# Optimization experiments

Hardware: AMD Instinct MI355X
Metric: run time of the kernel (lower is better)

The kernel has to match this reference:

```python
import jax, jax.numpy as jnp
import numpy as np

N_NODES = 200000
MAX_DEG = 128
S1, S2 = 25, 10  # neighbor sample sizes per hop (GraphSAGE defaults)


def setup_inputs() -> dict:
    key = jax.random.key(0)
    ks = jax.random.split(key, 9)
    F, H, C, B = 256, 128, 41, 1024
    return {
        "node_ids": jax.random.randint(ks[0], (B,), 0, N_NODES, dtype=jnp.int32),
        "features": jax.random.normal(ks[1], (N_NODES, F), dtype=jnp.float32),
        "adj_info": jax.random.randint(ks[2], (N_NODES, MAX_DEG), 0, N_NODES, dtype=jnp.int32),
        "W_self1": jax.random.normal(ks[3], (F, H), dtype=jnp.float32) * 0.05,
        "W_neigh1": jax.random.normal(ks[4], (F, H), dtype=jnp.float32) * 0.05,
        "W_self2": jax.random.normal(ks[5], (2 * H, H), dtype=jnp.float32) * 0.05,
        "W_neigh2": jax.random.normal(ks[6], (2 * H, H), dtype=jnp.float32) * 0.05,
        "W_pred": jax.random.normal(ks[7], (2 * H, C), dtype=jnp.float32) * 0.05,
        "b_pred": jnp.zeros((C,), dtype=jnp.float32),
    }


def _sample(adj_info, node_ids):
    """Uniform neighbor sampling: hop1 [B,S1], hop2 [B,S1,S2]."""
    k1, k2 = jax.random.split(jax.random.key(42))
    B = node_ids.shape[0]
    cols1 = jax.random.randint(k1, (B, S1), 0, MAX_DEG)
    hop1 = jnp.take_along_axis(adj_info[node_ids], cols1, axis=1)  # [B,S1]
    cols2 = jax.random.randint(k2, (B * S1, S2), 0, MAX_DEG)
    hop2 = jnp.take_along_axis(adj_info[hop1.reshape(-1)], cols2, axis=1)
    return hop1, hop2.reshape(B, S1, S2)


def _mean_agg(self_f, neigh_f, Ws, Wn, act):
    # GraphSAGE MeanAggregator with concat: [self@Ws ; mean(neigh)@Wn]
    neigh = neigh_f.mean(axis=-2)
    return act(jnp.concatenate([self_f @ Ws, neigh @ Wn], axis=-1))


def reference(node_ids, features, adj_info, W_self1, W_neigh1, W_self2, W_neigh2, W_pred, b_pred):
    hop1, hop2 = _sample(adj_info, node_ids)
    f0 = features[node_ids]      # [B,F]
    f1 = features[hop1]          # [B,S1,F]
    f2 = features[hop2]          # [B,S1,S2,F]

    h0 = _mean_agg(f0, f1, W_self1, W_neigh1, jax.nn.relu)   # [B,2H]
    h1 = _mean_agg(f1, f2, W_self1, W_neigh1, jax.nn.relu)   # [B,S1,2H]
    h = _mean_agg(h0, h1, W_self2, W_neigh2, lambda x: x)    # [B,2H]

    # tf.math.l2_normalize(x, 1): x * rsqrt(max(sum(x^2), 1e-12))
    h = h * jax.lax.rsqrt(jnp.maximum(jnp.sum(h * h, axis=1, keepdims=True), 1e-12))
    logits = h @ W_pred + b_pred
    return jax.nn.softmax(logits, axis=-1)
```

## Files before the change

### kernel.cpp

```cpp
#include <hip/hip_runtime.h>
#include <cstdint>
#include <cstddef>

#define BATCH 1024
#define S1 25
#define S2 10
#define FDIM 256
#define HDIM 128
#define NCLS 41
#define MAXDEG 128

typedef __attribute__((ext_vector_type(8))) short bf16x8;
typedef __attribute__((ext_vector_type(4))) float f32x4;

__host__ __device__ static inline void tf2x32(uint32_t k0, uint32_t k1,
                                              uint32_t c0, uint32_t c1,
                                              uint32_t& o0, uint32_t& o1) {
  const uint32_t ks2 = k0 ^ k1 ^ 0x1BD11BDAu;
  uint32_t x0 = c0 + k0, x1 = c1 + k1;
#define TFR(r) { x0 += x1; x1 = (x1 << (r)) | (x1 >> (32 - (r))); x1 ^= x0; }
  TFR(13) TFR(15) TFR(26) TFR(6)
  x0 += k1;  x1 += ks2 + 1u;
  TFR(17) TFR(29) TFR(16) TFR(24)
  x0 += ks2; x1 += k0 + 2u;
  TFR(13) TFR(15) TFR(26) TFR(6)
  x0 += k0;  x1 += k1 + 3u;
  TFR(17) TFR(29) TFR(16) TFR(24)
  x0 += k1;  x1 += ks2 + 4u;
  TFR(13) TFR(15) TFR(26) TFR(6)
  x0 += ks2; x1 += k0 + 5u;
#undef TFR
  o0 = x0; o1 = x1;
}

__device__ static inline uint32_t rand_bits_at(uint32_t kb0, uint32_t kb1, uint32_t j) {
  uint32_t o0, o1;
  tf2x32(kb0, kb1, 0u, j, o0, o1);
  return o0 ^ o1;
}

__device__ static inline ushort f2bf(float x) {
  uint32_t u = __float_as_uint(x);
  return (ushort)((u + 0x7fffu + ((u >> 16) & 1u)) >> 16);
}

__global__ __launch_bounds__(256)
void wprep_kernel(const float* __restrict__ Ws1, const float* __restrict__ Wn1,
                  ushort* __restrict__ WbT) {
  const int idx = blockIdx.x;
  const int h = idx >> 7, n = idx & 127;
  const float* W = h ? Wn1 : Ws1;
  WbT[(size_t)idx * FDIM + threadIdx.x] = f2bf(W[(size_t)threadIdx.x * HDIM + n]);
}

__global__ __launch_bounds__(256, 3)
void mega_kernel(const int* __restrict__ node_ids, const float* __restrict__ feat,
                 const int* __restrict__ adj, const ushort* __restrict__ WbT,
                 const float* __restrict__ Ws1, const float* __restrict__ Wn1,
                 const float* __restrict__ Ws2, const float* __restrict__ Wn2,
                 const float* __restrict__ Wp, const float* __restrict__ bp,
                 float* __restrict__ out,
                 uint32_t kb1_0, uint32_t kb1_1, uint32_t kb2_0, uint32_t kb2_1) {
  const int b = blockIdx.x;
  const int t = threadIdx.x;
  const int wave = t >> 6, lane = t & 63;
  const int lq = lane >> 4, lr = lane & 15;

  __shared__ int    hop1s[S1];
  __shared__ int    hop2s[S1 * S2];
  __shared__ ushort As0[8][32][40];
  __shared__ ushort As1[8][32][40];
  __shared__ float  F0[FDIM];
  __shared__ float  N1[4][FDIM];
  __shared__ float  H1M[2 * HDIM];
  __shared__ float  H0[2 * HDIM];
  __shared__ float  HN[2 * HDIM];
  __shared__ float  red[4];
  __shared__ float  lg[NCLS];
  __shared__ float  smx[2];

  const int nid = node_ids[b];

  if (t < S1) {
    uint32_t c1 = rand_bits_at(kb1_0, kb1_1, (uint32_t)(b * S1 + t)) & (MAXDEG - 1);
    hop1s[t] = adj[(size_t)nid * MAXDEG + c1];
  }
  __syncthreads();

  if (t < S1 * S2) {
    const int s1 = t / S2, j = t - s1 * S2;
    uint32_t c2 = rand_bits_at(kb2_0, kb2_1, (uint32_t)((b * S1 + s1) * S2 + j)) & (MAXDEG - 1);
    hop2s[t] = adj[(size_t)hop1s[s1] * MAXDEG + c2];
  }
  if (t < 64) ((float4*)F0)[t] = ((const float4*)(feat + (size_t)nid * FDIM))[t];
  {
    ushort4 z; z.x = 0; z.y = 0; z.z = 0; z.w = 0;
    for (int i = t; i < 448; i += 256) {
      const int rc = i >> 3, q = i & 7;
      const int r = 25 + (rc >> 3), ch = rc & 7;
      *(ushort4*)&As0[ch][r][q * 4] = z;
      *(ushort4*)&As1[ch][r][q * 4] = z;
    }
  }
  __syncthreads();

  {
    float ax = 0.f, ay = 0.f, az = 0.f, aw = 0.f;
    for (int s1 = wave; s1 < S1; s1 += 4) {
      const int rid1 = hop1s[s1];
      float4 v = ((const float4*)(feat + (size_t)rid1 * FDIM))[lane];
      float bx = 0.f, by = 0.f, bz = 0.f, bw = 0.f;
#pragma unroll
      for (int r = 0; r < S2; ++r) {
        const int rid = hop2s[s1 * S2 + r];
        float4 w = ((const float4*)(feat + (size_t)rid * FDIM))[lane];
        bx += w.x; by += w.y; bz += w.z; bw += w.w;
      }
      ax += v.x; ay += v.y; az += v.z; aw += v.w;
      ushort4 o1;
      o1.x = f2bf(v.x); o1.y = f2bf(v.y); o1.z = f2bf(v.z); o1.w = f2bf(v.w);
      *(ushort4*)&As0[lane >> 3][s1][(lane & 7) * 4] = o1;
      const float inv2 = 1.f / S2;
      ushort4 o2;
      o2.x = f2bf(bx * inv2); o2.y = f2bf(by * inv2);
      o2.z = f2bf(bz * inv2); o2.w = f2bf(bw * inv2);
      *(ushort4*)&As1[lane >> 3][s1][(lane & 7) * 4] = o2;
    }
    float4 p; p.x = ax; p.y = ay; p.z = az; p.w = aw;
    ((float4*)N1[wave])[lane] = p;
  }
  __syncthreads();

  {
    const float s = N1[0][t] + N1[1][t] + N1[2][t] + N1[3][t];
    N1[0][t] = s * (1.f / S1);
  }

#pragma unroll 1
  for (int half = 0; half < 2; ++half) {
    const ushort* Bmat = WbT + (size_t)half * HDIM * FDIM;
    const ushort (*As)[32][40] = half ? As1 : As0;

    bf16x8 bfr[2][8];
#pragma unroll
    for (int ct = 0; ct < 2; ++ct)
#pragma unroll
      for (int k0 = 0; k0 < 8; ++k0)
        bfr[ct][k0] = *(const bf16x8*)(Bmat + (size_t)(wave * 32 + ct * 16 + lr) * FDIM
                                       + k0 * 32 + lq * 8);

    f32x4 acc[2][2];
#pragma unroll
    for (int rt = 0; rt < 2; ++rt)
#pragma unroll
      for (int ct = 0; ct < 2; ++ct) acc[rt][ct] = (f32x4)(0.f);

#pragma unroll
    for (int k0 = 0; k0 < 8; ++k0) {
      bf16x8 af0 = *(const bf16x8*)&As[k0][lr][lq * 8];
      bf16x8 af1 = *(const bf16x8*)&As[k0][16 + lr][lq * 8];
#pragma unroll
      for (int ct = 0; ct < 2; ++ct) {
        acc[0][ct] = __builtin_amdgcn_mfma_f32_16x16x32_bf16(af0, bfr[ct][k0], acc[0][ct], 0, 0, 0);
        acc[1][ct] = __builtin_amdgcn_mfma_f32_16x16x32_bf16(af1, bfr[ct][k0], acc[1][ct], 0, 0, 0);
      }
    }

#pragma unroll
    for (int ct = 0; ct < 2; ++ct) {
      float s = 0.f;
#pragma unroll
      for (int rt = 0; rt < 2; ++rt)
#pragma unroll
        for (int r = 0; r < 4; ++r)
          s += fmaxf(acc[rt][ct][r], 0.f);
      s += __shfl_xor(s, 16, 64);
      s += __shfl_xor(s, 32, 64);
      if (lq == 0) H1M[half * HDIM + wave * 32 + ct * 16 + lr] = s * (1.f / S1);
    }
  }
  __syncthreads();

  const int hh = t >> 7, c = t & 127;
  {
    const float* W = hh ? Wn1 : Ws1;
    const float* Ap = hh ? N1[0] : F0;
    float acc = 0.f;
#pragma unroll 4
    for (int k4 = 0; k4 < 64; ++k4) {
      float4 a = ((const float4*)Ap)[k4];
      acc += a.x * W[(size_t)(k4 * 4 + 0) * HDIM + c]
           + a.y * W[(size_t)(k4 * 4 + 1) * HDIM + c]
           + a.z * W[(size_t)(k4 * 4 + 2) * HDIM + c]
           + a.w * W[(size_t)(k4 * 4 + 3) * HDIM + c];
    }
    H0[t] = fmaxf(acc, 0.f);
  }
  __syncthreads();

  float hv;
  {
    const float* W = hh ? Wn2 : Ws2;
    const float* Ap = hh ? H1M : H0;
    float acc = 0.f;
#pragma unroll 4
    for (int k4 = 0; k4 < 64; ++k4) {
      float4 a = ((const float4*)Ap)[k4];
      acc += a.x * W[(size_t)(k4 * 4 + 0) * HDIM + c]
           + a.y * W[(size_t)(k4 * 4 + 1) * HDIM + c]
           + a.z * W[(size_t)(k4 * 4 + 2) * HDIM + c]
           + a.w * W[(size_t)(k4 * 4 + 3) * HDIM + c];
    }
    hv = acc;
  }

  {
    float s = hv * hv;
#pragma unroll
    for (int off = 32; off; off >>= 1) s += __shfl_xor(s, off, 64);
    if (lane == 0) red[wave] = s;
  }
  __syncthreads();
  {
    const float scl = rsqrtf(fmaxf(red[0] + red[1] + red[2] + red[3], 1e-12f));
    HN[t] = hv * scl;
  }
  __syncthreads();

  {
    const int g = t >> 2, q = t & 3;
    if (g < NCLS) {
      float s = 0.f;
#pragma unroll 8
      for (int k = 0; k < 64; ++k)
        s += HN[q * 64 + k] * Wp[(size_t)(q * 64 + k) * NCLS + g];
      s += __shfl_xor(s, 1, 64);
      s += __shfl_xor(s, 2, 64);
      if (q == 0) lg[g] = s + bp[g];
    }
  }
  __syncthreads();
  if (t == 0) {
    float m = -1e30f;
    for (int i = 0; i < NCLS; ++i) m = fmaxf(m, lg[i]);
    float ssum = 0.f;
    for (int i = 0; i < NCLS; ++i) ssum += expf(lg[i] - m);
    smx[0] = m; smx[1] = ssum;
  }
  __syncthreads();
  if (t < NCLS)
    out[(size_t)b * NCLS + t] = expf(lg[t] - smx[0]) / smx[1];
}

extern "C" void kernel_launch(void* const* d_in, const int* in_sizes, int n_in,
                              void* d_out, int out_size, void* d_ws, size_t ws_size,
                              hipStream_t stream) {
  const int*   node_ids = (const int*)d_in[0];
  const float* features = (const float*)d_in[1];
  const int*   adj      = (const int*)d_in[2];
  const float* Ws1      = (const float*)d_in[3];
  const float* Wn1      = (const float*)d_in[4];
  const float* Ws2      = (const float*)d_in[5];
  const float* Wn2      = (const float*)d_in[6];
  const float* Wp       = (const float*)d_in[7];
  const float* bp       = (const float*)d_in[8];
  float* out = (float*)d_out;

  ushort* WbT = (ushort*)d_ws;

  uint32_t k1_0, k1_1, k2_0, k2_1, kb1_0, kb1_1, kb2_0, kb2_1;
  tf2x32(0u, 42u, 0u, 0u, k1_0, k1_1);
  tf2x32(0u, 42u, 0u, 1u, k2_0, k2_1);
  tf2x32(k1_0, k1_1, 0u, 1u, kb1_0, kb1_1);
  tf2x32(k2_0, k2_1, 0u, 1u, kb2_0, kb2_1);

  wprep_kernel<<<256, 256, 0, stream>>>(Ws1, Wn1, WbT);

  mega_kernel<<<BATCH, 256, 0, stream>>>(node_ids, features, adj, WbT,
                                         Ws1, Wn1, Ws2, Wn2, Wp, bp, out,
                                         kb1_0, kb1_1, kb2_0, kb2_1);
}
```

Measured before the change: 380.2 us.

## Share one LDS tile across MFMA halves to raise occupancy, merge sampling phases

Replaces the two bf16 LDS staging tiles with a single shared tile. The neighbor-mean operands are held in registers and written into that tile only after the self half of the MFMA finishes. B fragments are now loaded per k-step rather than preloaded, and launch bounds go from 3 to 5 blocks per CU so more blocks fit on each CU. The two-hop sampling is merged into one phase with one less barrier, and the dense-layer loops use a larger unroll. This costs an extra barrier between the MFMA halves, more live registers for the held operands, and a possible spill under the tighter register budget.

```diff
diff --git a/kernel.cpp b/kernel.cpp
--- a/kernel.cpp
+++ b/kernel.cpp
@@ -53,7 +53,43 @@
   WbT[(size_t)idx * FDIM + threadIdx.x] = f2bf(W[(size_t)threadIdx.x * HDIM + n]);
 }
 
-__global__ __launch_bounds__(256, 3)
+__device__ static inline void mfma_half(const ushort (*As)[32][40],
+                                        const ushort* __restrict__ Bmat,
+                                        float* __restrict__ dst,
+                                        int wave, int lq, int lr) {
+  f32x4 acc[2][2];
+#pragma unroll
+  for (int rt = 0; rt < 2; ++rt)
+#pragma unroll
+    for (int ct = 0; ct < 2; ++ct) acc[rt][ct] = (f32x4)(0.f);
+
+#pragma unroll
+  for (int k0 = 0; k0 < 8; ++k0) {
+    bf16x8 b0 = *(const bf16x8*)(Bmat + (size_t)(wave * 32 + lr) * FDIM + k0 * 32 + lq * 8);
+    bf16x8 b1 = *(const bf16x8*)(Bmat + (size_t)(wave * 32 + 16 + lr) * FDIM + k0 * 32 + lq * 8);
+    bf16x8 a0 = *(const bf16x8*)&As[k0][lr][lq * 8];
+    bf16x8 a1 = *(const bf16x8*)&As[k0][16 + lr][lq * 8];
+    acc[0][0] = __builtin_amdgcn_mfma_f32_16x16x32_bf16(a0, b0, acc[0][0], 0, 0, 0);
+    acc[0][1] = __builtin_amdgcn_mfma_f32_16x16x32_bf16(a0, b1, acc[0][1], 0, 0, 0);
+    acc[1][0] = __builtin_amdgcn_mfma_f32_16x16x32_bf16(a1, b0, acc[1][0], 0, 0, 0);
+    acc[1][1] = __builtin_amdgcn_mfma_f32_16x16x32_bf16(a1, b1, acc[1][1], 0, 0, 0);
+  }
+
+#pragma unroll
+  for (int ct = 0; ct < 2; ++ct) {
+    float s = 0.f;
+#pragma unroll
+    for (int rt = 0; rt < 2; ++rt)
+#pragma unroll
+      for (int r = 0; r < 4; ++r)
+        s += fmaxf(acc[rt][ct][r], 0.f);
+    s += __shfl_xor(s, 16, 64);
+    s += __shfl_xor(s, 32, 64);
+    if (lq == 0) dst[wave * 32 + ct * 16 + lr] = s * (1.f / S1);
+  }
+}
+
+__global__ __launch_bounds__(256, 5)
 void mega_kernel(const int* __restrict__ node_ids, const float* __restrict__ feat,
                  const int* __restrict__ adj, const ushort* __restrict__ WbT,
                  const float* __restrict__ Ws1, const float* __restrict__ Wn1,
@@ -68,8 +104,7 @@
 
   __shared__ int    hop1s[S1];
   __shared__ int    hop2s[S1 * S2];
-  __shared__ ushort As0[8][32][40];
-  __shared__ ushort As1[8][32][40];
+  __shared__ ushort As[8][32][40];
   __shared__ float  F0[FDIM];
   __shared__ float  N1[4][FDIM];
   __shared__ float  H1M[2 * HDIM];
@@ -81,16 +116,13 @@
 
   const int nid = node_ids[b];
 
-  if (t < S1) {
-    uint32_t c1 = rand_bits_at(kb1_0, kb1_1, (uint32_t)(b * S1 + t)) & (MAXDEG - 1);
-    hop1s[t] = adj[(size_t)nid * MAXDEG + c1];
-  }
-  __syncthreads();
-
   if (t < S1 * S2) {
-    const int s1 = t / S2, j = t - s1 * S2;
-    uint32_t c2 = rand_bits_at(kb2_0, kb2_1, (uint32_t)((b * S1 + s1) * S2 + j)) & (MAXDEG - 1);
-    hop2s[t] = adj[(size_t)hop1s[s1] * MAXDEG + c2];
+    const int s1 = t / S2;
+    uint32_t c1 = rand_bits_at(kb1_0, kb1_1, (uint32_t)(b * S1 + s1)) & (MAXDEG - 1);
+    const int h1 = adj[(size_t)nid * MAXDEG + c1];
+    if (t == s1 * S2) hop1s[s1] = h1;
+    uint32_t c2 = rand_bits_at(kb2_0, kb2_1, (uint32_t)(b * S1 * S2 + t)) & (MAXDEG - 1);
+    hop2s[t] = adj[(size_t)h1 * MAXDEG + c2];
   }
   if (t < 64) ((float4*)F0)[t] = ((const float4*)(feat + (size_t)nid * FDIM))[t];
   {
@@ -98,87 +130,58 @@
     for (int i = t; i < 448; i += 256) {
       const int rc = i >> 3, q = i & 7;
       const int r = 25 + (rc >> 3), ch = rc & 7;
-      *(ushort4*)&As0[ch][r][q * 4] = z;
-      *(ushort4*)&As1[ch][r][q * 4] = z;
-    }
-  }
-  __syncthreads();
-
+      *(ushort4*)&As[ch][r][q * 4] = z;
+    }
+  }
+  __syncthreads();
+
+  ushort4 nm[7];
   {
     float ax = 0.f, ay = 0.f, az = 0.f, aw = 0.f;
-    for (int s1 = wave; s1 < S1; s1 += 4) {
-      const int rid1 = hop1s[s1];
-      float4 v = ((const float4*)(feat + (size_t)rid1 * FDIM))[lane];
-      float bx = 0.f, by = 0.f, bz = 0.f, bw = 0.f;
-#pragma unroll
-      for (int r = 0; r < S2; ++r) {
-        const int rid = hop2s[s1 * S2 + r];
-        float4 w = ((const float4*)(feat + (size_t)rid * FDIM))[lane];
-        bx += w.x; by += w.y; bz += w.z; bw += w.w;
+#pragma unroll
+    for (int i = 0; i < 7; ++i) {
+      const int s1 = wave + i * 4;
+      if (s1 < S1) {
+        const int rid1 = hop1s[s1];
+        float4 v = ((const float4*)(feat + (size_t)rid1 * FDIM))[lane];
+        float bx = 0.f, by = 0.f, bz = 0.f, bw = 0.f;
+#pragma unroll
+        for (int r = 0; r < S2; ++r) {
+          const int rid = hop2s[s1 * S2 + r];
+          float4 w = ((const float4*)(feat + (size_t)rid * FDIM))[lane];
+          bx += w.x; by += w.y; bz += w.z; bw += w.w;
+        }
+        ax += v.x; ay += v.y; az += v.z; aw += v.w;
+        ushort4 o1;
+        o1.x = f2bf(v.x); o1.y = f2bf(v.y); o1.z = f2bf(v.z); o1.w = f2bf(v.w);
+        *(ushort4*)&As[lane >> 3][s1][(lane & 7) * 4] = o1;
+        const float inv2 = 1.f / S2;
+        ushort4 o2;
+        o2.x = f2bf(bx * inv2); o2.y = f2bf(by * inv2);
+        o2.z = f2bf(bz * inv2); o2.w = f2bf(bw * inv2);
+        nm[i] = o2;
       }
-      ax += v.x; ay += v.y; az += v.z; aw += v.w;
-      ushort4 o1;
-      o1.x = f2bf(v.x); o1.y = f2bf(v.y); o1.z = f2bf(v.z); o1.w = f2bf(v.w);
-      *(ushort4*)&As0[lane >> 3][s1][(lane & 7) * 4] = o1;
-      const float inv2 = 1.f / S2;
-      ushort4 o2;
-      o2.x = f2bf(bx * inv2); o2.y = f2bf(by * inv2);
-      o2.z = f2bf(bz * inv2); o2.w = f2bf(bw * inv2);
-      *(ushort4*)&As1[lane >> 3][s1][(lane & 7) * 4] = o2;
     }
     float4 p; p.x = ax; p.y = ay; p.z = az; p.w = aw;
     ((float4*)N1[wave])[lane] = p;
   }
   __syncthreads();
 
+  mfma_half(As, WbT, H1M, wave, lq, lr);
+  __syncthreads();
+
+#pragma unroll
+  for (int i = 0; i < 7; ++i) {
+    const int s1 = wave + i * 4;
+    if (s1 < S1) *(ushort4*)&As[lane >> 3][s1][(lane & 7) * 4] = nm[i];
+  }
   {
     const float s = N1[0][t] + N1[1][t] + N1[2][t] + N1[3][t];
     N1[0][t] = s * (1.f / S1);
   }
-
-#pragma unroll 1
-  for (int half = 0; half < 2; ++half) {
-    const ushort* Bmat = WbT + (size_t)half * HDIM * FDIM;
-    const ushort (*As)[32][40] = half ? As1 : As0;
-
-    bf16x8 bfr[2][8];
-#pragma unroll
-    for (int ct = 0; ct < 2; ++ct)
-#pragma unroll
-      for (int k0 = 0; k0 < 8; ++k0)
-        bfr[ct][k0] = *(const bf16x8*)(Bmat + (size_t)(wave * 32 + ct * 16 + lr) * FDIM
-                                       + k0 * 32 + lq * 8);
-
-    f32x4 acc[2][2];
-#pragma unroll
-    for (int rt = 0; rt < 2; ++rt)
-#pragma unroll
-      for (int ct = 0; ct < 2; ++ct) acc[rt][ct] = (f32x4)(0.f);
-
-#pragma unroll
-    for (int k0 = 0; k0 < 8; ++k0) {
-      bf16x8 af0 = *(const bf16x8*)&As[k0][lr][lq * 8];
-      bf16x8 af1 = *(const bf16x8*)&As[k0][16 + lr][lq * 8];
-#pragma unroll
-      for (int ct = 0; ct < 2; ++ct) {
-        acc[0][ct] = __builtin_amdgcn_mfma_f32_16x16x32_bf16(af0, bfr[ct][k0], acc[0][ct], 0, 0, 0);
-        acc[1][ct] = __builtin_amdgcn_mfma_f32_16x16x32_bf16(af1, bfr[ct][k0], acc[1][ct], 0, 0, 0);
-      }
-    }
-
-#pragma unroll
-    for (int ct = 0; ct < 2; ++ct) {
-      float s = 0.f;
-#pragma unroll
-      for (int rt = 0; rt < 2; ++rt)
-#pragma unroll
-        for (int r = 0; r < 4; ++r)
-          s += fmaxf(acc[rt][ct][r], 0.f);
-      s += __shfl_xor(s, 16, 64);
-      s += __shfl_xor(s, 32, 64);
-      if (lq == 0) H1M[half * HDIM + wave * 32 + ct * 16 + lr] = s * (1.f / S1);
-    }
-  }
+  __syncthreads();
+
+  mfma_half(As, WbT + (size_t)HDIM * FDIM, H1M + HDIM, wave, lq, lr);
   __syncthreads();
 
   const int hh = t >> 7, c = t & 127;
@@ -186,7 +189,7 @@
     const float* W = hh ? Wn1 : Ws1;
     const float* Ap = hh ? N1[0] : F0;
     float acc = 0.f;
-#pragma unroll 4
+#pragma unroll 8
     for (int k4 = 0; k4 < 64; ++k4) {
       float4 a = ((const float4*)Ap)[k4];
       acc += a.x * W[(size_t)(k4 * 4 + 0) * HDIM + c]
@@ -203,7 +206,7 @@
     const float* W = hh ? Wn2 : Ws2;
     const float* Ap = hh ? H1M : H0;
     float acc = 0.f;
-#pragma unroll 4
+#pragma unroll 8
     for (int k4 = 0; k4 < 64; ++k4) {
       float4 a = ((const float4*)Ap)[k4];
       acc += a.x * W[(size_t)(k4 * 4 + 0) * HDIM + c]
```

After: 404.3 us. 6.3% more time.
